# Kernel optimization log

Measured on AMD Instinct MI355X. Metric: run time of the kernel, lower is better.

## Reference

```python
import jax, jax.numpy as jnp
import numpy as np
import math

B, N, D, O, H = 2, 3072, 64, 64, 4

def setup_inputs() -> dict:
    key = jax.random.key(0)
    ks = jax.random.split(key, 8)
    x = jax.random.normal(ks[0], (B, N, D), dtype=jnp.float32)
    edge_index = jax.random.randint(ks[1], (B, N, N), 0, 2, dtype=jnp.int32)
    s = 1.0 / math.sqrt(D)
    Wv = jax.random.uniform(ks[2], (H, D, O), jnp.float32, -s, s)
    bv = jax.random.uniform(ks[3], (H, O), jnp.float32, -s, s)
    Wq = jax.random.uniform(ks[4], (H, D, O), jnp.float32, -s, s)
    bq = jax.random.uniform(ks[5], (H, O), jnp.float32, -s, s)
    Wk = jax.random.uniform(ks[6], (H, D, O), jnp.float32, -s, s)
    bk = jax.random.uniform(ks[7], (H, O), jnp.float32, -s, s)
    return {"x": x, "edge_index": edge_index, "Wv": Wv, "bv": bv,
            "Wq": Wq, "bq": bq, "Wk": Wk, "bk": bk}

def reference(x, edge_index, Wv, bv, Wq, bq, Wk, bk):
    # x: [B,N,D]; edge_index: dense {0,1} adjacency [B,N,N]
    dk = jnp.asarray(math.sqrt(x.shape[-1]), x.dtype)
    v = jnp.einsum('bnd,hdo->bhno', x, Wv) + bv[None, :, None, :]
    q = jnp.einsum('bnd,hdo->bhno', x, Wq) + bq[None, :, None, :]
    k = jnp.einsum('bnd,hdo->bhno', x, Wk) + bk[None, :, None, :]
    scores = jnp.einsum('bhno,bhmo->bhnm', q, k) / dk        # [B,H,N,N]
    scores = jax.nn.leaky_relu(scores, 0.2)
    mask = (-1e10) * (1.0 - edge_index.astype(scores.dtype))  # [B,N,N]
    scores = scores + mask[:, None, :, :]
    prop = jax.nn.softmax(scores, axis=-1)
    # dropout on v omitted (inference mode: identity)
    feats = jnp.einsum('bhnm,bhmo->bhno', prop, v)            # [B,H,N,O]
    out = jnp.mean(feats, axis=1)                             # [B,N,O]
    return jax.nn.leaky_relu(out, 0.2)
```

## Files before the change

kernel.cpp:

```cpp
#include <hip/hip_runtime.h>
#include <hip/hip_bf16.h>
#include <cstdint>

#define Bc 2
#define Nc 3072
#define Hc 4
#define NW32 96
#define TILEB 8192
#define KSC 4
#define TPS (NW32/KSC)

typedef __bf16    bf16x8 __attribute__((ext_vector_type(8)));
typedef _Float16  f16x8  __attribute__((ext_vector_type(8)));
typedef float     f32x16 __attribute__((ext_vector_type(16)));

#define QSCALE 0.18033688f

static __device__ __forceinline__ f32x16 mfma32bf(bf16x8 a, bf16x8 b, f32x16 c) {
    return __builtin_amdgcn_mfma_f32_32x32x16_bf16(a, b, c, 0, 0, 0);
}
static __device__ __forceinline__ f32x16 mfma32h(f16x8 a, f16x8 b, f32x16 c) {
    return __builtin_amdgcn_mfma_f32_32x32x16_f16(a, b, c, 0, 0, 0);
}
static __device__ __forceinline__ uint32_t pkrtz(float lo, float hi) {
    uint32_t w;
    asm("v_cvt_pkrtz_f16_f32 %0, %1, %2" : "=v"(w) : "v"(lo), "v"(hi));
    return w;
}

static __device__ __forceinline__ void softmax_pack(const f32x16& sc, uint32_t mwh,
                                                    uint32_t W8[8], float& lsum)
{
    #pragma unroll
    for (int i = 0; i < 8; ++i) {
        const int bp0 = (2*i & 3) + 8*(2*i >> 2);
        float s0 = sc[2*i], s1 = sc[2*i + 1];
        float a0 = fmaxf(s0, 0.2f*s0);
        float a1 = fmaxf(s1, 0.2f*s1);
        float e0, e1;
        asm("v_exp_f32 %0, %1" : "=v"(e0) : "v"(a0));
        asm("v_exp_f32 %0, %1" : "=v"(e1) : "v"(a1));
        uint32_t m0 = (uint32_t)(((int)(mwh << (31 - bp0))) >> 31);
        uint32_t m1 = (uint32_t)(((int)(mwh << (30 - bp0))) >> 31);
        float p0 = __uint_as_float(__float_as_uint(e0) & m0);
        float p1 = __uint_as_float(__float_as_uint(e1) & m1);
        lsum += p0 + p1;
        W8[i] = pkrtz(p0, p1);
    }
}

static __device__ __forceinline__ void assemble_pa(uint32_t W8[8], f16x8& pa0, f16x8& pa1)
{
    uint32_t a0 = W8[0], a2 = W8[2], a1 = W8[1], a3 = W8[3];
    uint32_t b0 = W8[4], b2 = W8[6], b1 = W8[5], b3 = W8[7];
    asm("v_permlane32_swap_b32 %0, %1" : "+v"(a0), "+v"(a2));
    asm("v_permlane32_swap_b32 %0, %1" : "+v"(a1), "+v"(a3));
    asm("v_permlane32_swap_b32 %0, %1" : "+v"(b0), "+v"(b2));
    asm("v_permlane32_swap_b32 %0, %1" : "+v"(b1), "+v"(b3));
    union { uint32_t u[4]; f16x8 v; } u0, u1;
    u0.u[0] = a0; u0.u[1] = a1; u0.u[2] = a2; u0.u[3] = a3;
    u1.u[0] = b0; u1.u[1] = b1; u1.u[2] = b2; u1.u[3] = b3;
    pa0 = u0.v; pa1 = u1.v;
}

static __device__ __forceinline__ void load_subtile(const char* gt, int hi, int l31,
                                                    f16x8 (&K)[4], f16x8 (&V)[4])
{
    #pragma unroll
    for (int kk = 0; kk < 4; ++kk)
        K[kk] = *(const f16x8*)(gt + ((kk*2 + hi) << 9) + (l31 << 4));
    #pragma unroll
    for (int i = 0; i < 4; ++i) {
        const int kkp = i >> 1, ot = i & 1;
        V[i] = *(const f16x8*)(gt + 4096 + ((kkp*2 + hi) << 10) + ((ot*32 + l31) << 4));
    }
}

static __device__ __forceinline__ void compute_subtile(
    const f16x8 (&K)[4], const f16x8 (&V)[4], uint32_t mw, int hi,
    const f16x8 (&qf)[4], const f32x16& fzero,
    f32x16& acc0, f32x16& acc1, float& lsum)
{
    f32x16 sc;
    __builtin_amdgcn_s_setprio(1);
    sc = mfma32h(K[0], qf[0], fzero);
    sc = mfma32h(K[1], qf[1], sc);
    sc = mfma32h(K[2], qf[2], sc);
    sc = mfma32h(K[3], qf[3], sc);
    __builtin_amdgcn_s_setprio(0);

    uint32_t W8[8];
    softmax_pack(sc, mw >> (hi*4), W8, lsum);
    f16x8 pa0, pa1;
    assemble_pa(W8, pa0, pa1);

    __builtin_amdgcn_s_setprio(1);
    acc0 = mfma32h(pa0, V[0], acc0);
    acc1 = mfma32h(pa0, V[1], acc1);
    acc0 = mfma32h(pa1, V[2], acc0);
    acc1 = mfma32h(pa1, V[3], acc1);
    __builtin_amdgcn_s_setprio(0);
}

__global__ void prep_kernel(const float* __restrict__ Wq, const float* __restrict__ Wk,
                            const float* __restrict__ Wv,
                            const float* __restrict__ bq, const float* __restrict__ bk,
                            const float* __restrict__ bv,
                            __bf16* __restrict__ Wbh, __bf16* __restrict__ Wbl,
                            float* __restrict__ Bs)
{
    int i = blockIdx.x*256 + threadIdx.x;
    int d = i & 63, o = (i >> 6) & 63, h = (i >> 12) & 3, p = i >> 14;
    const float* W = (p == 0) ? Wq : (p == 1) ? Wk : Wv;
    float scale = (p == 0) ? QSCALE : 1.0f;
    float val = W[(h*64 + d)*64 + o] * scale;
    int idx = (((p*Hc + h)*64 + o) << 6) + d;
    __bf16 hi = (__bf16)val;
    Wbh[idx] = hi;
    Wbl[idx] = (__bf16)(val - (float)hi);
    if (i < 3*Hc*64) {
        int pp = i / (Hc*64), rest = i % (Hc*64);
        const float* B = (pp == 0) ? bq : (pp == 1) ? bk : bv;
        Bs[i] = B[rest] * ((pp == 0) ? QSCALE : 1.0f);
    }
}

__global__ __launch_bounds__(256) void qkv_mfma(
    const float* __restrict__ x,
    const __bf16* __restrict__ Wbh, const __bf16* __restrict__ Wbl,
    const float* __restrict__ Bs,
    _Float16* __restrict__ Qf, _Float16* __restrict__ Kf,
    _Float16* __restrict__ KVimg)
{
    const int lane = threadIdx.x & 63, w = threadIdx.x >> 6;
    const int l31 = lane & 31, hi = lane >> 5;
    int t = blockIdx.x;
    int nt = t % 48; t /= 48;
    int b  = t & 1;  t >>= 1;
    int p  = t % 3;
    int h  = t / 3;
    const int r0 = (w >> 1)*32, c0 = (w & 1)*32, n0 = nt*64;

    bf16x8 xh[4], xl[4], wh[4], wl[4];
    #pragma unroll
    for (int kk = 0; kk < 4; ++kk) {
        size_t xoff = (((size_t)(b*Nc + n0 + r0 + l31)) << 6) + kk*16 + hi*8;
        float4 f0 = *(const float4*)(x + xoff);
        float4 f1 = *(const float4*)(x + xoff + 4);
        float xs[8] = {f0.x, f0.y, f0.z, f0.w, f1.x, f1.y, f1.z, f1.w};
        #pragma unroll
        for (int j = 0; j < 8; ++j) {
            __bf16 hh = (__bf16)xs[j];
            xh[kk][j] = hh;
            xl[kk][j] = (__bf16)(xs[j] - (float)hh);
        }
        size_t woff = (((size_t)((p*Hc + h)*64 + c0 + l31)) << 6) + kk*16 + hi*8;
        wh[kk] = *(const bf16x8*)(Wbh + woff);
        wl[kk] = *(const bf16x8*)(Wbl + woff);
    }
    float bias = Bs[(p*Hc + h)*64 + c0 + l31];
    f32x16 acc;
    #pragma unroll
    for (int i = 0; i < 16; ++i) acc[i] = bias;
    #pragma unroll
    for (int kk = 0; kk < 4; ++kk) {
        acc = mfma32bf(xh[kk], wh[kk], acc);
        acc = mfma32bf(xl[kk], wh[kk], acc);
        acc = mfma32bf(xh[kk], wl[kk], acc);
    }
    const int bh = b*Hc + h;
    if (p < 2) {
        _Float16* dst = (p == 0) ? Qf : Kf;
        #pragma unroll
        for (int r = 0; r < 16; ++r) {
            int row = (r & 3) + 8*(r >> 2) + 4*hi;
            size_t idx = (((size_t)bh*Nc + n0 + r0 + row) << 6) + c0 + l31;
            dst[idx] = (_Float16)acc[r];
        }
    } else {
        const int t_img = (n0 + r0) >> 5;
        char* img = (char*)KVimg + (size_t)(bh*96 + t_img)*TILEB;
        #pragma unroll
        for (int grp = 0; grp < 2; ++grp) {
            uint32_t wH[4];
            #pragma unroll
            for (int j = 0; j < 4; ++j)
                wH[j] = pkrtz(acc[grp*8 + 2*j], acc[grp*8 + 2*j + 1]);
            asm("v_permlane32_swap_b32 %0, %1" : "+v"(wH[0]), "+v"(wH[2]));
            asm("v_permlane32_swap_b32 %0, %1" : "+v"(wH[1]), "+v"(wH[3]));
            const int kb = grp*2 + hi;
            const int o  = c0 + l31;
            uint4 gh = {wH[0], wH[1], wH[2], wH[3]};
            *(uint4*)(img + 4096 + ((kb*64 + o) << 4)) = gh;
        }
    }
}

__global__ void imgk_kernel(const _Float16* __restrict__ Kf, _Float16* __restrict__ KVimg)
{
    const int t = blockIdx.x % 96, bh = blockIdx.x / 96;
    char* img = (char*)KVimg + (size_t)(bh*96 + t)*TILEB;
    int dc = threadIdx.x & 7, key = threadIdx.x >> 3;
    size_t src = (((size_t)bh*Nc + t*32 + key) << 6) + dc*8;
    *(uint4*)(img + (dc*32 + key)*16) = *(const uint4*)(Kf + src);
}

__global__ void pack_kernel(const int* __restrict__ edge, uint32_t* __restrict__ pmT)
{
    int gw = blockIdx.x*4 + (threadIdx.x >> 6);
    int lane = threadIdx.x & 63;
    int ng = gw % 48; gw /= 48;
    int w  = gw % NW32; gw /= NW32;
    int b  = gw;
    int n = ng*64 + lane;
    const uint4* ep = (const uint4*)(edge + ((size_t)b*Nc + n)*Nc + w*32);
    uint32_t word = 0;
    #pragma unroll
    for (int i = 0; i < 8; ++i) {
        uint4 e = ep[i];
        word |= (e.x ? 1u : 0u) << (4*i);
        word |= (e.y ? 1u : 0u) << (4*i + 1);
        word |= (e.z ? 1u : 0u) << (4*i + 2);
        word |= (e.w ? 1u : 0u) << (4*i + 3);
    }
    pmT[((size_t)b*NW32 + w)*Nc + n] = word;
}

__global__ __launch_bounds__(256, 3) void attn_mfma(
    const _Float16* __restrict__ Qf,
    const _Float16* __restrict__ KVimg, const uint32_t* __restrict__ pmT,
    float* __restrict__ PA, float* __restrict__ PL)
{
    const int lane = threadIdx.x & 63, w = threadIdx.x >> 6;
    const int l31 = lane & 31, hi = lane >> 5;
    int gb = blockIdx.x;
    const int bh = gb & 7; gb >>= 3;
    const int qt = gb % 24;
    const int ks = gb / 24;
    const int b = bh >> 2;
    const int qrow0 = qt*128 + w*32;
    const int t0 = ks*TPS;

    const uint32_t* pmp = pmT + ((size_t)b*NW32 + t0)*Nc + qrow0 + l31;
    const char* gt = (const char*)KVimg + (size_t)(bh*96 + t0)*TILEB;

    f16x8 qf[4];
    #pragma unroll
    for (int kk = 0; kk < 4; ++kk) {
        size_t qoff = (((size_t)bh*Nc + qrow0 + l31) << 6) + kk*16 + hi*8;
        qf[kk] = *(const f16x8*)(Qf + qoff);
    }
    f32x16 fzero;
    #pragma unroll
    for (int i = 0; i < 16; ++i) fzero[i] = 0.f;

    f32x16 acc0 = fzero, acc1 = fzero;
    float lsum = 0.f;

    f16x8 KA[4], VA[4], KB[4], VB[4];
    uint32_t mwA, mwB;
    load_subtile(gt, hi, l31, KA, VA);
    mwA = pmp[0];

    #pragma unroll 1
    for (int j = 0; j < TPS/2; ++j) {
        load_subtile(gt + (size_t)(2*j + 1)*TILEB, hi, l31, KB, VB);
        mwB = pmp[(size_t)(2*j + 1)*Nc];
        compute_subtile(KA, VA, mwA, hi, qf, fzero, acc0, acc1, lsum);
        const int tn = (2*j + 2 < TPS) ? (2*j + 2) : 0;
        load_subtile(gt + (size_t)tn*TILEB, hi, l31, KA, VA);
        mwA = pmp[(size_t)tn*Nc];
        compute_subtile(KB, VB, mwB, hi, qf, fzero, acc0, acc1, lsum);
    }

    lsum += __shfl_xor(lsum, 32);
    float* po = PA + (((size_t)(bh*KSC + ks)*Nc + qrow0) << 6);
    #pragma unroll
    for (int r = 0; r < 16; ++r) {
        int row = (r & 3) + 8*(r >> 2) + 4*hi;
        po[((size_t)row << 6) + l31]      = acc0[r];
        po[((size_t)row << 6) + 32 + l31] = acc1[r];
    }
    if (lane < 32)
        PL[(size_t)(bh*KSC + ks)*Nc + qrow0 + l31] = lsum;
}

__global__ void merge_kernel(const float* __restrict__ PA, const float* __restrict__ PL,
                             float* __restrict__ out)
{
    int gid = blockIdx.x*256 + threadIdx.x;
    int o  = gid & 63;
    int bn = gid >> 6;
    int n  = bn % Nc;
    int b  = bn / Nc;
    float ft = 0.f;
    for (int h = 0; h < Hc; ++h) {
        int bh = b*Hc + h;
        float A = 0.f, L = 0.f;
        for (int ks = 0; ks < KSC; ++ks) {
            A += PA[(((size_t)(bh*KSC + ks)*Nc + n) << 6) + o];
            L += PL[(size_t)(bh*KSC + ks)*Nc + n];
        }
        ft += A / L;
    }
    ft *= 0.25f;
    out[((size_t)bn << 6) + o] = fmaxf(ft, 0.f) + 0.2f*fminf(ft, 0.f);
}

extern "C" void kernel_launch(void* const* d_in, const int* in_sizes, int n_in,
                              void* d_out, int out_size, void* d_ws, size_t ws_size,
                              hipStream_t stream)
{
    const float* x    = (const float*)d_in[0];
    const int*   edge = (const int*)d_in[1];
    const float* Wv   = (const float*)d_in[2];
    const float* bv   = (const float*)d_in[3];
    const float* Wq   = (const float*)d_in[4];
    const float* bq   = (const float*)d_in[5];
    const float* Wk   = (const float*)d_in[6];
    const float* bk   = (const float*)d_in[7];
    float* out = (float*)d_out;

    const size_t PROJ = (size_t)Bc*Hc*Nc*64;
    char* p = (char*)d_ws;
    __bf16* Wbh = (__bf16*)p;     p += 49152*2;
    __bf16* Wbl = (__bf16*)p;     p += 49152*2;
    float*  Bs  = (float*)p;      p += 4096;
    _Float16* Qf = (_Float16*)p;  p += PROJ*2;
    _Float16* Kf = (_Float16*)p;  p += PROJ*2;
    _Float16* KVimg = (_Float16*)p; p += (size_t)Bc*Hc*96*TILEB;
    uint32_t* pmT = (uint32_t*)p; p += (size_t)Bc*NW32*Nc*4;
    float* PA = (float*)p;        p += (size_t)Bc*Hc*KSC*Nc*64*4;
    float* PL = (float*)p;

    hipLaunchKernelGGL(prep_kernel, dim3(192),  dim3(256), 0, stream,
                       Wq, Wk, Wv, bq, bk, bv, Wbh, Wbl, Bs);
    hipLaunchKernelGGL(qkv_mfma,    dim3(1152), dim3(256), 0, stream,
                       x, Wbh, Wbl, Bs, Qf, Kf, KVimg);
    hipLaunchKernelGGL(imgk_kernel, dim3(Bc*Hc*96), dim3(256), 0, stream, Kf, KVimg);
    hipLaunchKernelGGL(pack_kernel, dim3(Bc*NW32*48/4), dim3(256), 0, stream, edge, pmT);
    hipLaunchKernelGGL(attn_mfma,   dim3(8*KSC*24), dim3(256), 0, stream,
                       Qf, KVimg, pmT, PA, PL);
    hipLaunchKernelGGL(merge_kernel, dim3((Bc*Nc*64)/256), dim3(256), 0, stream,
                       PA, PL, out);
}
```

Measured before the change: 78.65 us.

## Double key-split count, fuse weight prep with mask packing, use dot2 row sums

The key dimension of attention is split into 8 chunks instead of 4, giving the attention kernel twice as many blocks with half the tiles each. This improves occupancy and parallelism at the cost of larger partial buffers and more merge work. The weight-prep and adjacency bit-packing kernels are merged into one launch to save a kernel launch. In the softmax, the exponentials are packed to fp16 before masking, and the row sum is accumulated with v_dot2_f32_f16 against a vector of ones. This trims VALU work but sums the rounded fp16 values rather than the fp32 ones.

```diff
diff --git a/kernel.cpp b/kernel.cpp
--- a/kernel.cpp
+++ b/kernel.cpp
@@ -7,7 +7,7 @@
 #define Hc 4
 #define NW32 96
 #define TILEB 8192
-#define KSC 4
+#define KSC 8
 #define TPS (NW32/KSC)
 
 typedef __bf16    bf16x8 __attribute__((ext_vector_type(8)));
@@ -29,7 +29,8 @@
 }
 
 static __device__ __forceinline__ void softmax_pack(const f32x16& sc, uint32_t mwh,
-                                                    uint32_t W8[8], float& lsum)
+                                                    uint32_t W8[8], float& lsum,
+                                                    uint32_t ones32)
 {
     #pragma unroll
     for (int i = 0; i < 8; ++i) {
@@ -40,12 +41,12 @@
         float e0, e1;
         asm("v_exp_f32 %0, %1" : "=v"(e0) : "v"(a0));
         asm("v_exp_f32 %0, %1" : "=v"(e1) : "v"(a1));
+        uint32_t pk = pkrtz(e0, e1);
         uint32_t m0 = (uint32_t)(((int)(mwh << (31 - bp0))) >> 31);
         uint32_t m1 = (uint32_t)(((int)(mwh << (30 - bp0))) >> 31);
-        float p0 = __uint_as_float(__float_as_uint(e0) & m0);
-        float p1 = __uint_as_float(__float_as_uint(e1) & m1);
-        lsum += p0 + p1;
-        W8[i] = pkrtz(p0, p1);
+        uint32_t wv = pk & ((m0 & 0x0000ffffu) | (m1 & 0xffff0000u));
+        W8[i] = wv;
+        asm("v_dot2_f32_f16 %0, %1, %2, %0" : "+v"(lsum) : "v"(wv), "v"(ones32));
     }
 }
 
@@ -78,7 +79,7 @@
 
 static __device__ __forceinline__ void compute_subtile(
     const f16x8 (&K)[4], const f16x8 (&V)[4], uint32_t mw, int hi,
-    const f16x8 (&qf)[4], const f32x16& fzero,
+    const f16x8 (&qf)[4], const f32x16& fzero, uint32_t ones32,
     f32x16& acc0, f32x16& acc1, float& lsum)
 {
     f32x16 sc;
@@ -90,7 +91,7 @@
     __builtin_amdgcn_s_setprio(0);
 
     uint32_t W8[8];
-    softmax_pack(sc, mw >> (hi*4), W8, lsum);
+    softmax_pack(sc, mw >> (hi*4), W8, lsum, ones32);
     f16x8 pa0, pa1;
     assemble_pa(W8, pa0, pa1);
 
@@ -102,26 +103,47 @@
     __builtin_amdgcn_s_setprio(0);
 }
 
-__global__ void prep_kernel(const float* __restrict__ Wq, const float* __restrict__ Wk,
-                            const float* __restrict__ Wv,
-                            const float* __restrict__ bq, const float* __restrict__ bk,
-                            const float* __restrict__ bv,
-                            __bf16* __restrict__ Wbh, __bf16* __restrict__ Wbl,
-                            float* __restrict__ Bs)
-{
-    int i = blockIdx.x*256 + threadIdx.x;
-    int d = i & 63, o = (i >> 6) & 63, h = (i >> 12) & 3, p = i >> 14;
-    const float* W = (p == 0) ? Wq : (p == 1) ? Wk : Wv;
-    float scale = (p == 0) ? QSCALE : 1.0f;
-    float val = W[(h*64 + d)*64 + o] * scale;
-    int idx = (((p*Hc + h)*64 + o) << 6) + d;
-    __bf16 hi = (__bf16)val;
-    Wbh[idx] = hi;
-    Wbl[idx] = (__bf16)(val - (float)hi);
-    if (i < 3*Hc*64) {
-        int pp = i / (Hc*64), rest = i % (Hc*64);
-        const float* B = (pp == 0) ? bq : (pp == 1) ? bk : bv;
-        Bs[i] = B[rest] * ((pp == 0) ? QSCALE : 1.0f);
+__global__ void preppack_kernel(const float* __restrict__ Wq, const float* __restrict__ Wk,
+                                const float* __restrict__ Wv,
+                                const float* __restrict__ bq, const float* __restrict__ bk,
+                                const float* __restrict__ bv,
+                                const int* __restrict__ edge,
+                                __bf16* __restrict__ Wbh, __bf16* __restrict__ Wbl,
+                                float* __restrict__ Bs, uint32_t* __restrict__ pmT)
+{
+    if (blockIdx.x < 192) {
+        int i = blockIdx.x*256 + threadIdx.x;
+        int d = i & 63, o = (i >> 6) & 63, h = (i >> 12) & 3, p = i >> 14;
+        const float* W = (p == 0) ? Wq : (p == 1) ? Wk : Wv;
+        float scale = (p == 0) ? QSCALE : 1.0f;
+        float val = W[(h*64 + d)*64 + o] * scale;
+        int idx = (((p*Hc + h)*64 + o) << 6) + d;
+        __bf16 hi = (__bf16)val;
+        Wbh[idx] = hi;
+        Wbl[idx] = (__bf16)(val - (float)hi);
+        if (i < 3*Hc*64) {
+            int pp = i / (Hc*64), rest = i % (Hc*64);
+            const float* B = (pp == 0) ? bq : (pp == 1) ? bk : bv;
+            Bs[i] = B[rest] * ((pp == 0) ? QSCALE : 1.0f);
+        }
+    } else {
+        int gw = (blockIdx.x - 192)*4 + (threadIdx.x >> 6);
+        int lane = threadIdx.x & 63;
+        int ng = gw % 48; gw /= 48;
+        int w  = gw % NW32; gw /= NW32;
+        int b  = gw;
+        int n = ng*64 + lane;
+        const uint4* ep = (const uint4*)(edge + ((size_t)b*Nc + n)*Nc + w*32);
+        uint32_t word = 0;
+        #pragma unroll
+        for (int i = 0; i < 8; ++i) {
+            uint4 e = ep[i];
+            word |= (e.x ? 1u : 0u) << (4*i);
+            word |= (e.y ? 1u : 0u) << (4*i + 1);
+            word |= (e.z ? 1u : 0u) << (4*i + 2);
+            word |= (e.w ? 1u : 0u) << (4*i + 3);
+        }
+        pmT[((size_t)b*NW32 + w)*Nc + n] = word;
     }
 }
 
@@ -205,27 +227,6 @@
     *(uint4*)(img + (dc*32 + key)*16) = *(const uint4*)(Kf + src);
 }
 
-__global__ void pack_kernel(const int* __restrict__ edge, uint32_t* __restrict__ pmT)
-{
-    int gw = blockIdx.x*4 + (threadIdx.x >> 6);
-    int lane = threadIdx.x & 63;
-    int ng = gw % 48; gw /= 48;
-    int w  = gw % NW32; gw /= NW32;
-    int b  = gw;
-    int n = ng*64 + lane;
-    const uint4* ep = (const uint4*)(edge + ((size_t)b*Nc + n)*Nc + w*32);
-    uint32_t word = 0;
-    #pragma unroll
-    for (int i = 0; i < 8; ++i) {
-        uint4 e = ep[i];
-        word |= (e.x ? 1u : 0u) << (4*i);
-        word |= (e.y ? 1u : 0u) << (4*i + 1);
-        word |= (e.z ? 1u : 0u) << (4*i + 2);
-        word |= (e.w ? 1u : 0u) << (4*i + 3);
-    }
-    pmT[((size_t)b*NW32 + w)*Nc + n] = word;
-}
-
 __global__ __launch_bounds__(256, 3) void attn_mfma(
     const _Float16* __restrict__ Qf,
     const _Float16* __restrict__ KVimg, const uint32_t* __restrict__ pmT,
@@ -253,6 +254,7 @@
     f32x16 fzero;
     #pragma unroll
     for (int i = 0; i < 16; ++i) fzero[i] = 0.f;
+    const uint32_t ones32 = 0x3C003C00u;
 
     f32x16 acc0 = fzero, acc1 = fzero;
     float lsum = 0.f;
@@ -266,11 +268,11 @@
     for (int j = 0; j < TPS/2; ++j) {
         load_subtile(gt + (size_t)(2*j + 1)*TILEB, hi, l31, KB, VB);
         mwB = pmp[(size_t)(2*j + 1)*Nc];
-        compute_subtile(KA, VA, mwA, hi, qf, fzero, acc0, acc1, lsum);
+        compute_subtile(KA, VA, mwA, hi, qf, fzero, ones32, acc0, acc1, lsum);
         const int tn = (2*j + 2 < TPS) ? (2*j + 2) : 0;
         load_subtile(gt + (size_t)tn*TILEB, hi, l31, KA, VA);
         mwA = pmp[(size_t)tn*Nc];
-        compute_subtile(KB, VB, mwB, hi, qf, fzero, acc0, acc1, lsum);
+        compute_subtile(KB, VB, mwB, hi, qf, fzero, ones32, acc0, acc1, lsum);
     }
 
     lsum += __shfl_xor(lsum, 32);
@@ -333,12 +335,11 @@
     float* PA = (float*)p;        p += (size_t)Bc*Hc*KSC*Nc*64*4;
     float* PL = (float*)p;
 
-    hipLaunchKernelGGL(prep_kernel, dim3(192),  dim3(256), 0, stream,
-                       Wq, Wk, Wv, bq, bk, bv, Wbh, Wbl, Bs);
+    hipLaunchKernelGGL(preppack_kernel, dim3(192 + Bc*NW32*48/4), dim3(256), 0, stream,
+                       Wq, Wk, Wv, bq, bk, bv, edge, Wbh, Wbl, Bs, pmT);
     hipLaunchKernelGGL(qkv_mfma,    dim3(1152), dim3(256), 0, stream,
                        x, Wbh, Wbl, Bs, Qf, Kf, KVimg);
     hipLaunchKernelGGL(imgk_kernel, dim3(Bc*Hc*96), dim3(256), 0, stream, Kf, KVimg);
-    hipLaunchKernelGGL(pack_kernel, dim3(Bc*NW32*48/4), dim3(256), 0, stream, edge, pmT);
     hipLaunchKernelGGL(attn_mfma,   dim3(8*KSC*24), dim3(256), 0, stream,
                        Qf, KVimg, pmT, PA, PL);
     hipLaunchKernelGGL(merge_kernel, dim3((Bc*Nc*64)/256), dim3(256), 0, stream,
```

Result: no change. 78.86 us (+0.3%).
